# Performance work log

Measured on AMD Instinct MI355X. Metric: run time of the kernel, lower is better.

Reference implementation:

```python
import jax, jax.numpy as jnp
import numpy as np

K = 20          # knn neighbors (hard-coded default in source)
BN_EPS = 1e-3   # keras BatchNormalization default epsilon


def setup_inputs() -> dict:
    key = jax.random.key(0)
    ks = jax.random.split(key, 8)
    B, N, D = 8, 4096, 64
    x = jax.random.normal(ks[0], (B, N, D), dtype=jnp.float32)
    # Conv1D(kernel_size=1) == pointwise dense over feature dim
    w1 = jax.random.normal(ks[1], (2 * D, 32), dtype=jnp.float32) * 0.05
    b1 = jnp.zeros((32,), dtype=jnp.float32)
    g1 = jnp.ones((32,), dtype=jnp.float32)
    be1 = jnp.zeros((32,), dtype=jnp.float32)
    w2 = jax.random.normal(ks[2], (32, 64), dtype=jnp.float32) * 0.05
    b2 = jnp.zeros((64,), dtype=jnp.float32)
    g2 = jnp.ones((64,), dtype=jnp.float32)
    be2 = jnp.zeros((64,), dtype=jnp.float32)
    wd = jax.random.normal(ks[3], (64, N), dtype=jnp.float32) * 0.05
    bd = jnp.zeros((N,), dtype=jnp.float32)
    return {"x": x, "w1": w1, "b1": b1, "g1": g1, "be1": be1,
            "w2": w2, "b2": b2, "g2": g2, "be2": be2, "wd": wd, "bd": bd}


def _batchnorm(h, gamma, beta):
    # batch-stat normalization over (batch, points) axes, like BN(momentum=0) in training
    mean = jnp.mean(h, axis=(0, 1), keepdims=True)
    var = jnp.var(h, axis=(0, 1), keepdims=True)
    return gamma * (h - mean) * jax.lax.rsqrt(var + BN_EPS) + beta


def reference(x, w1, b1, g1, be1, w2, b2, g2, be2, wd, bd):
    B, N, D = x.shape
    # pairwise squared L2 distance: ||a||^2 - 2 a.b + ||b||^2  -> (B, N, N)
    inner = jnp.einsum('bnd,bmd->bnm', x, x)
    sq = jnp.sum(jnp.square(x), axis=-1, keepdims=True)  # (B, N, 1)
    adj = sq - 2.0 * inner + jnp.swapaxes(sq, 1, 2)
    # KNN: top-k of negative distance
    _, knn_idx = jax.lax.top_k(-adj, K)                   # (B, N, K)
    # gather neighbor features (B, N, K, D)
    neighbors = jax.vmap(lambda xf, idx: xf[idx])(x, knn_idx)
    central = x[:, :, None, :]                            # (B, N, 1, D)
    edge = jnp.concatenate(
        [jnp.broadcast_to(central, (B, N, K, D)), neighbors - central], axis=-1)
    feat = jnp.max(edge, axis=2)                          # (B, N, 2D)
    h = jax.nn.relu(feat @ w1 + b1)
    h = _batchnorm(h, g1, be1)
    h = jax.nn.relu(h @ w2 + b2)
    h = _batchnorm(h, g2, be2)
    pooled = jnp.max(h, axis=1)                           # (B, 64)
    return jax.nn.softmax(pooled @ wd + bd, axis=-1)      # (B, N)
```

## Files before the change

### kernel.cpp

```cpp
#include <hip/hip_runtime.h>
#include <stdint.h>

#define N_PTS 4096
#define B_SZ 8
#define D_DIM 64
#define KNN 20
#define NROWS (B_SZ * N_PTS)
#define H1C 32
#define H2C 64
#define BN_EPS 1e-3f
#define NSLICE 2
#define SLICE_C (N_PTS / NSLICE)
#define NT (SLICE_C / 64)

typedef __attribute__((ext_vector_type(8))) short bf16x8;
typedef __attribute__((ext_vector_type(4))) float f32x4;
typedef unsigned long long ull;

__device__ __forceinline__ ushort f2bf(float f) {
    uint32_t u = __float_as_uint(f);
    uint32_t r = (u + 0x7fffu + ((u >> 16) & 1u)) >> 16;
    return (ushort)r;
}
__device__ __forceinline__ float bf2f(ushort h) {
    return __uint_as_float(((uint32_t)h) << 16);
}

__device__ __forceinline__ void ins20(ull (&k)[KNN], ull cur) {
#pragma unroll
    for (int p = KNN - 1; p >= 1; --p) {
        bool c = cur < k[p - 1];
        ull t = (k[p] < cur) ? k[p] : cur;
        k[p] = c ? k[p - 1] : t;
    }
    k[0] = (k[0] < cur) ? k[0] : cur;
}

__global__ void prep_kernel(const float* __restrict__ x, ushort* __restrict__ xh,
                            ushort* __restrict__ xl, float* __restrict__ sq) {
    int row = blockIdx.x * blockDim.x + threadIdx.x;
    if (row >= NROWS) return;
    const float4* xr = (const float4*)(x + (size_t)row * D_DIM);
    ushort4* ho = (ushort4*)(xh + (size_t)row * D_DIM);
    ushort4* lo = (ushort4*)(xl + (size_t)row * D_DIM);
    float acc = 0.f;
#pragma unroll
    for (int q = 0; q < 16; ++q) {
        float4 v = xr[q];
        acc = fmaf(v.x, v.x, acc);
        acc = fmaf(v.y, v.y, acc);
        acc = fmaf(v.z, v.z, acc);
        acc = fmaf(v.w, v.w, acc);
        ushort4 h, l;
        h.x = f2bf(v.x); l.x = f2bf(v.x - bf2f(h.x));
        h.y = f2bf(v.y); l.y = f2bf(v.y - bf2f(h.y));
        h.z = f2bf(v.z); l.z = f2bf(v.z - bf2f(h.z));
        h.w = f2bf(v.w); l.w = f2bf(v.w - bf2f(h.w));
        ho[q] = h; lo[q] = l;
    }
    sq[row] = acc;
}

__global__ __launch_bounds__(256, 4) void dist_topk(
    const ushort* __restrict__ xh, const ushort* __restrict__ xl,
    const float* __restrict__ sq, ull* __restrict__ part) {
    int tid = threadIdx.x;
    int lane = tid & 63;
    int w = tid >> 6;
    int blk = blockIdx.x & 63;
    int b = blockIdx.x >> 6;
    int slice = blockIdx.y;
    const ushort* xhb = xh + (size_t)b * N_PTS * D_DIM;
    const ushort* xlb = xl + (size_t)b * N_PTS * D_DIM;
    const float* sqb = sq + (size_t)b * N_PTS;

    int qr0 = blk * 64 + w * 16;
    int fr = lane & 15;
    int fg = lane >> 4;

    bf16x8 q_h[2], q_l[2];
    {
        const ushort* ph = xhb + (size_t)(qr0 + fr) * D_DIM + fg * 8;
        const ushort* pl = xlb + (size_t)(qr0 + fr) * D_DIM + fg * 8;
        q_h[0] = *(const bf16x8*)(ph);
        q_h[1] = *(const bf16x8*)(ph + 32);
        q_l[0] = *(const bf16x8*)(pl);
        q_l[1] = *(const bf16x8*)(pl + 32);
    }
    float sqi = sqb[qr0 + fr];

    ull k20[KNN];
#pragma unroll
    for (int p = 0; p < KNN; ++p) k20[p] = ~0ull;
    ull b0 = ~0ull, b1 = ~0ull, b2 = ~0ull, b3 = ~0ull;
    ull b4 = ~0ull, b5 = ~0ull, b6 = ~0ull, b7 = ~0ull;
    int cnt = 0;
    unsigned thr = 0xFFFFFFFFu;

    int cbase = slice * SLICE_C;
    const ushort* pah = xhb + (size_t)(cbase + fr) * D_DIM + fg * 8;
    const ushort* pal = xlb + (size_t)(cbase + fr) * D_DIM + fg * 8;
    const float* psq = sqb + cbase + fg * 4;

    for (int t = 0; t < NT; ++t) {
        int c0 = cbase + t * 64;
#pragma unroll
        for (int s = 0; s < 4; ++s) {
            int cc = c0 + s * 16;
            bf16x8 a_h0 = *(const bf16x8*)(pah + s * 16 * D_DIM);
            bf16x8 a_h1 = *(const bf16x8*)(pah + s * 16 * D_DIM + 32);
            bf16x8 a_l0 = *(const bf16x8*)(pal + s * 16 * D_DIM);
            bf16x8 a_l1 = *(const bf16x8*)(pal + s * 16 * D_DIM + 32);
            float4 sqj = *(const float4*)(psq + s * 16);
            f32x4 accA = {0.f, 0.f, 0.f, 0.f};
            f32x4 accB = {0.f, 0.f, 0.f, 0.f};
            accA = __builtin_amdgcn_mfma_f32_16x16x32_bf16(a_h0, q_h[0], accA, 0, 0, 0);
            accB = __builtin_amdgcn_mfma_f32_16x16x32_bf16(a_h0, q_l[0], accB, 0, 0, 0);
            accA = __builtin_amdgcn_mfma_f32_16x16x32_bf16(a_h1, q_h[1], accA, 0, 0, 0);
            accB = __builtin_amdgcn_mfma_f32_16x16x32_bf16(a_h1, q_l[1], accB, 0, 0, 0);
            accB = __builtin_amdgcn_mfma_f32_16x16x32_bf16(a_l0, q_h[0], accB, 0, 0, 0);
            accB = __builtin_amdgcn_mfma_f32_16x16x32_bf16(a_l1, q_h[1], accB, 0, 0, 0);
            float sqjv[4] = {sqj.x, sqj.y, sqj.z, sqj.w};
#pragma unroll
            for (int qq = 0; qq < 4; ++qq) {
                float base = sqi + sqjv[qq];
                float d = fmaf(-2.f, accA[qq], fmaf(-2.f, accB[qq], base));
                d = fmaxf(d, 0.f);
                unsigned u = __float_as_uint(d);
                if (u <= thr) {
                    b7 = b6; b6 = b5; b5 = b4; b4 = b3;
                    b3 = b2; b2 = b1; b1 = b0;
                    b0 = (((ull)u) << 32) | (unsigned)(cc + fg * 4 + qq);
                    ++cnt;
                }
            }
            if (__any(cnt >= 5)) {
                ull e;
                e = (cnt >= 1) ? b0 : ~0ull; ins20(k20, e);
                e = (cnt >= 2) ? b1 : ~0ull; ins20(k20, e);
                e = (cnt >= 3) ? b2 : ~0ull; ins20(k20, e);
                e = (cnt >= 4) ? b3 : ~0ull; ins20(k20, e);
                e = (cnt >= 5) ? b4 : ~0ull; ins20(k20, e);
                if (__any(cnt >= 6)) {
                    e = (cnt >= 6) ? b5 : ~0ull; ins20(k20, e);
                    e = (cnt >= 7) ? b6 : ~0ull; ins20(k20, e);
                    e = (cnt >= 8) ? b7 : ~0ull; ins20(k20, e);
                }
                cnt = 0;
                unsigned t5  = (unsigned)(k20[4]  >> 32);
                unsigned t20 = (unsigned)(k20[19] >> 32);
                unsigned o;
                o = __shfl_xor(t5, 16);  t5  = (o > t5)  ? o : t5;
                o = __shfl_xor(t5, 32);  t5  = (o > t5)  ? o : t5;
                o = __shfl_xor(t20, 16); t20 = (o < t20) ? o : t20;
                o = __shfl_xor(t20, 32); t20 = (o < t20) ? o : t20;
                thr = (t5 < t20) ? t5 : t20;
            }
        }
        pah += 64 * D_DIM;
        pal += 64 * D_DIM;
        psq += 64;
    }
    if (__any(cnt >= 1)) {
        ull e;
        e = (cnt >= 1) ? b0 : ~0ull; ins20(k20, e);
        e = (cnt >= 2) ? b1 : ~0ull; ins20(k20, e);
        if (__any(cnt >= 3)) {
            e = (cnt >= 3) ? b2 : ~0ull; ins20(k20, e);
            e = (cnt >= 4) ? b3 : ~0ull; ins20(k20, e);
        }
    }

#pragma unroll
    for (int g = 1; g < 4; ++g) {
        for (int p = 0; p < KNN; ++p) {
            ull key = __shfl(k20[p], fr + 16 * g);
            bool useful = (lane < 16) && (key < k20[KNN - 1]);
            if (!__any(useful ? 1 : 0)) break;
            if (lane < 16) ins20(k20, key);
        }
    }
    if (lane < 16) {
        int grow = b * N_PTS + blk * 64 + w * 16 + lane;
#pragma unroll
        for (int p = 0; p < KNN; ++p)
            part[((size_t)(slice * KNN + p)) * NROWS + grow] = k20[p];
    }
}

__global__ void knn_merge(const ull* __restrict__ part, int* __restrict__ knn) {
    int row = blockIdx.x * blockDim.x + threadIdx.x;
    if (row >= NROWS) return;
    ull fin[KNN];
#pragma unroll
    for (int p = 0; p < KNN; ++p) fin[p] = part[(size_t)p * NROWS + row];
    for (int sl = 1; sl < NSLICE; ++sl) {
        for (int p = 0; p < KNN; ++p) {
            ull key = part[(size_t)(sl * KNN + p) * NROWS + row];
            if (key >= fin[KNN - 1]) break;
            ins20(fin, key);
        }
    }
#pragma unroll
    for (int q = 0; q < KNN; ++q)
        knn[(size_t)q * NROWS + row] = (int)(unsigned)(fin[q] & 0xffffffffu);
}

__global__ void edge_mlp1(const float* __restrict__ x, const int* __restrict__ knn,
                          const float* __restrict__ w1, const float* __restrict__ b1,
                          float* __restrict__ h1) {
    __shared__ float w1t[H1C][132];
    __shared__ float feat[4][128];
    int tid = threadIdx.x;
    int wave = tid >> 6, lane = tid & 63;
    for (int idx = tid; idx < 128 * H1C; idx += 256) {
        int f = idx >> 5, c = idx & 31;
        w1t[c][f] = w1[idx];
    }
    int row = blockIdx.x * 4 + wave;
    int b = row >> 12;
    int n = row & (N_PTS - 1);
    const float* xb = x + (size_t)b * N_PTS * D_DIM;
    float central = xb[(size_t)n * D_DIM + lane];
    float m = -1e30f;
    for (int k = 0; k < KNN; ++k) {
        int j = knn[(size_t)k * NROWS + row];
        float xn = xb[(size_t)j * D_DIM + lane];
        m = fmaxf(m, xn - central);
    }
    feat[wave][lane] = central;
    feat[wave][64 + lane] = m;
    __syncthreads();
    if (lane < H1C) {
        int c = lane;
        float acc = b1[c];
#pragma unroll
        for (int fq = 0; fq < 32; ++fq) {
            float4 fv = *(const float4*)(&feat[wave][fq * 4]);
            float4 wv = *(const float4*)(&w1t[c][fq * 4]);
            acc = fmaf(fv.x, wv.x, acc);
            acc = fmaf(fv.y, wv.y, acc);
            acc = fmaf(fv.z, wv.z, acc);
            acc = fmaf(fv.w, wv.w, acc);
        }
        h1[(size_t)row * H1C + c] = fmaxf(acc, 0.f);
    }
}

template <int CH>
__global__ void stats_kernel(const float* __restrict__ h, float* __restrict__ sum,
                             float* __restrict__ sumsq) {
    const int RPI = 256 / CH;
    int tid = threadIdx.x;
    int c = tid % CH;
    int r0 = tid / CH;
    float s = 0.f, s2 = 0.f;
    for (int r = blockIdx.x * RPI + r0; r < NROWS; r += gridDim.x * RPI) {
        float v = h[(size_t)r * CH + c];
        s += v;
        s2 = fmaf(v, v, s2);
    }
    __shared__ float ls[256], ls2[256];
    ls[tid] = s; ls2[tid] = s2;
    __syncthreads();
    for (int step = 128; step >= CH; step >>= 1) {
        if (tid < step) { ls[tid] += ls[tid + step]; ls2[tid] += ls2[tid + step]; }
        __syncthreads();
    }
    if (tid < CH) {
        atomicAdd(&sum[tid], ls[tid]);
        atomicAdd(&sumsq[tid], ls2[tid]);
    }
}

template <int CH>
__global__ void coeff_kernel(const float* sum, const float* sumsq, const float* g,
                             const float* be, float* a, float* cc) {
    int c = threadIdx.x;
    if (c >= CH) return;
    float mean = sum[c] * (1.f / NROWS);
    float var = sumsq[c] * (1.f / NROWS) - mean * mean;
    float aa = g[c] * rsqrtf(var + BN_EPS);
    a[c] = aa;
    cc[c] = be[c] - aa * mean;
}

__global__ void mlp2_kernel(const float* __restrict__ h1, const float* __restrict__ w2,
                            const float* __restrict__ b2, const float* __restrict__ a1,
                            const float* __restrict__ c1, float* __restrict__ h2) {
    __shared__ float w2s[H1C][H2C];
    __shared__ float hb[4][H1C];
    int tid = threadIdx.x;
    for (int idx = tid; idx < H1C * H2C; idx += 256)
        w2s[idx >> 6][idx & 63] = w2[idx];
    int rw = tid >> 6;
    int c = tid & 63;
    int row = blockIdx.x * 4 + rw;
    if (c < H1C) {
        float v = h1[(size_t)row * H1C + c];
        hb[rw][c] = fmaf(a1[c], v, c1[c]);
    }
    __syncthreads();
    float acc = b2[c];
#pragma unroll
    for (int f = 0; f < H1C; ++f)
        acc = fmaf(hb[rw][f], w2s[f][c], acc);
    h2[(size_t)row * H2C + c] = fmaxf(acc, 0.f);
}

__global__ void pool_part(const float* __restrict__ h2, float* __restrict__ pmax,
                          float* __restrict__ pmin) {
    int bb = blockIdx.x >> 6;
    int ch = blockIdx.x & 63;
    int tid = threadIdx.x;
    int rw = tid >> 6, c = tid & 63;
    float mx = -1e30f, mn = 1e30f;
    const float* hbase = h2 + (size_t)bb * N_PTS * H2C;
    for (int n = ch * 64 + rw; n < (ch + 1) * 64; n += 4) {
        float v = hbase[(size_t)n * H2C + c];
        mx = fmaxf(mx, v);
        mn = fminf(mn, v);
    }
    __shared__ float smx[256], smn[256];
    smx[tid] = mx; smn[tid] = mn;
    __syncthreads();
    if (tid < 128) { smx[tid] = fmaxf(smx[tid], smx[tid + 128]); smn[tid] = fminf(smn[tid], smn[tid + 128]); }
    __syncthreads();
    if (tid < 64) {
        pmax[((size_t)bb * 64 + ch) * 64 + tid] = fmaxf(smx[tid], smx[tid + 64]);
        pmin[((size_t)bb * 64 + ch) * 64 + tid] = fminf(smn[tid], smn[tid + 64]);
    }
}

__global__ void pool_final(const float* pmax, const float* pmin, const float* a2,
                           const float* c2, float* pooled) {
    int bb = blockIdx.x;
    int c = threadIdx.x;
    float M = -1e30f, m = 1e30f;
    for (int ch = 0; ch < 64; ++ch) {
        M = fmaxf(M, pmax[((size_t)bb * 64 + ch) * 64 + c]);
        m = fminf(m, pmin[((size_t)bb * 64 + ch) * 64 + c]);
    }
    float aa = a2[c];
    pooled[bb * 64 + c] = (aa >= 0.f) ? fmaf(aa, M, c2[c]) : fmaf(aa, m, c2[c]);
}

__global__ __launch_bounds__(256) void logits_kernel(const float* __restrict__ pooled,
                                                     const float* __restrict__ wd,
                                                     const float* __restrict__ bd,
                                                     float* __restrict__ lg) {
    __shared__ float pl[8][64];
    int tid = threadIdx.x;
    for (int i = tid; i < 8 * 64; i += 256) ((float*)pl)[i] = pooled[i];
    __syncthreads();
    int col = blockIdx.x * 64 + (tid & 63);
    int bg = tid >> 6;
    float acc0 = bd[col];
    float acc1 = acc0;
#pragma unroll
    for (int c = 0; c < 64; ++c) {
        float wv = wd[(size_t)c * N_PTS + col];
        acc0 = fmaf(pl[bg][c], wv, acc0);
        acc1 = fmaf(pl[bg + 4][c], wv, acc1);
    }
    lg[(size_t)bg * N_PTS + col] = acc0;
    lg[(size_t)(bg + 4) * N_PTS + col] = acc1;
}

__global__ __launch_bounds__(1024) void softmax_kernel(const float* __restrict__ lg,
                                                       float* __restrict__ out) {
    int bb = blockIdx.x;
    int tid = threadIdx.x;
    __shared__ float red[1024];
    float logit[4];
#pragma unroll
    for (int q = 0; q < 4; ++q)
        logit[q] = lg[(size_t)bb * N_PTS + tid + q * 1024];
    float mx = fmaxf(fmaxf(logit[0], logit[1]), fmaxf(logit[2], logit[3]));
    red[tid] = mx;
    __syncthreads();
    for (int s = 512; s >= 1; s >>= 1) {
        if (tid < s) red[tid] = fmaxf(red[tid], red[tid + s]);
        __syncthreads();
    }
    float gmax = red[0];
    __syncthreads();
    float e[4];
    float ssum = 0.f;
#pragma unroll
    for (int q = 0; q < 4; ++q) { e[q] = __expf(logit[q] - gmax); ssum += e[q]; }
    red[tid] = ssum;
    __syncthreads();
    for (int s = 512; s >= 1; s >>= 1) {
        if (tid < s) red[tid] += red[tid + s];
        __syncthreads();
    }
    float inv = 1.f / red[0];
#pragma unroll
    for (int q = 0; q < 4; ++q)
        out[(size_t)bb * N_PTS + tid + q * 1024] = e[q] * inv;
}

extern "C" void kernel_launch(void* const* d_in, const int* in_sizes, int n_in,
                              void* d_out, int out_size, void* d_ws, size_t ws_size,
                              hipStream_t stream) {
    (void)in_sizes; (void)n_in; (void)out_size; (void)ws_size;
    const float* x   = (const float*)d_in[0];
    const float* w1  = (const float*)d_in[1];
    const float* b1  = (const float*)d_in[2];
    const float* g1  = (const float*)d_in[3];
    const float* be1 = (const float*)d_in[4];
    const float* w2  = (const float*)d_in[5];
    const float* b2  = (const float*)d_in[6];
    const float* g2  = (const float*)d_in[7];
    const float* be2 = (const float*)d_in[8];
    const float* wd  = (const float*)d_in[9];
    const float* bd  = (const float*)d_in[10];

    char* ws = (char*)d_ws;
    size_t off = 0;
    auto alloc = [&](size_t bytes) -> void* {
        void* p = ws + off;
        off += (bytes + 255) & ~(size_t)255;
        return p;
    };
    ushort* xh = (ushort*)alloc((size_t)NROWS * D_DIM * 2);
    ushort* xl = (ushort*)alloc((size_t)NROWS * D_DIM * 2);
    float* sq = (float*)alloc((size_t)NROWS * 4);
    ull* part = (ull*)alloc((size_t)NROWS * NSLICE * KNN * 8);
    int* knn = (int*)alloc((size_t)NROWS * KNN * 4);
    float* h1 = (float*)alloc((size_t)NROWS * H1C * 4);
    float* h2 = (float*)alloc((size_t)NROWS * H2C * 4);
    float* stats = (float*)alloc(4096);
    float* pmax = (float*)alloc(8 * 64 * 64 * 4);
    float* pmin = (float*)alloc(8 * 64 * 64 * 4);
    float* pooled = (float*)alloc(8 * 64 * 4);
    float* lg = (float*)alloc((size_t)B_SZ * N_PTS * 4);

    float* sum1 = stats,       *sumsq1 = stats + 32, *a1 = stats + 64,  *c1 = stats + 96;
    float* sum2 = stats + 128, *sumsq2 = stats + 192, *a2 = stats + 256, *c2 = stats + 320;

    hipMemsetAsync(stats, 0, 4096, stream);

    prep_kernel<<<NROWS / 256, 256, 0, stream>>>(x, xh, xl, sq);
    dist_topk<<<dim3(B_SZ * 64, NSLICE), 256, 0, stream>>>(xh, xl, sq, part);
    knn_merge<<<NROWS / 256, 256, 0, stream>>>(part, knn);
    edge_mlp1<<<NROWS / 4, 256, 0, stream>>>(x, knn, w1, b1, h1);
    stats_kernel<H1C><<<256, 256, 0, stream>>>(h1, sum1, sumsq1);
    coeff_kernel<H1C><<<1, 32, 0, stream>>>(sum1, sumsq1, g1, be1, a1, c1);
    mlp2_kernel<<<NROWS / 4, 256, 0, stream>>>(h1, w2, b2, a1, c1, h2);
    stats_kernel<H2C><<<256, 256, 0, stream>>>(h2, sum2, sumsq2);
    coeff_kernel<H2C><<<1, 64, 0, stream>>>(sum2, sumsq2, g2, be2, a2, c2);
    pool_part<<<512, 256, 0, stream>>>(h2, pmax, pmin);
    pool_final<<<8, 64, 0, stream>>>(pmax, pmin, a2, c2, pooled);
    logits_kernel<<<64, 256, 0, stream>>>(pooled, wd, bd, lg);
    softmax_kernel<<<8, 1024, 0, stream>>>(lg, (float*)d_out);
}
```

Before: 431.2 us.

## Split candidate columns across waves within a block and merge top-k in LDS

Each block now handles 16 query rows, and its four waves each scan a quarter of the candidate points, where before each wave scanned half the points for its own rows. The per-row pruning threshold is shared through LDS via atomicMin, so one wave's progress tightens the filter for the others. The per-wave top-20 lists are merged in shared memory inside the kernel, which removes the separate knn_merge kernel and its global partial buffer. In exchange the candidate buffer is flushed on the first tile and each step reads the shared threshold, and there are four times as many blocks, each loading only 16 query rows.

```diff
diff --git a/kernel.cpp b/kernel.cpp
--- a/kernel.cpp
+++ b/kernel.cpp
@@ -9,8 +9,7 @@
 #define H1C 32
 #define H2C 64
 #define BN_EPS 1e-3f
-#define NSLICE 2
-#define SLICE_C (N_PTS / NSLICE)
+#define SLICE_C 1024
 #define NT (SLICE_C / 64)
 
 typedef __attribute__((ext_vector_type(8))) short bf16x8;
@@ -63,20 +62,24 @@
 
 __global__ __launch_bounds__(256, 4) void dist_topk(
     const ushort* __restrict__ xh, const ushort* __restrict__ xl,
-    const float* __restrict__ sq, ull* __restrict__ part) {
+    const float* __restrict__ sq, int* __restrict__ knn) {
+    __shared__ unsigned lthr[16];
+    __shared__ ull lists[4][16][KNN];
+
     int tid = threadIdx.x;
     int lane = tid & 63;
     int w = tid >> 6;
-    int blk = blockIdx.x & 63;
-    int b = blockIdx.x >> 6;
-    int slice = blockIdx.y;
+    int g = blockIdx.x;
+    int b = g >> 8;
+    int qr0 = (g & 255) * 16;
     const ushort* xhb = xh + (size_t)b * N_PTS * D_DIM;
     const ushort* xlb = xl + (size_t)b * N_PTS * D_DIM;
     const float* sqb = sq + (size_t)b * N_PTS;
 
-    int qr0 = blk * 64 + w * 16;
     int fr = lane & 15;
     int fg = lane >> 4;
+
+    if (tid < 16) lthr[tid] = 0xFFFFFFFFu;
 
     bf16x8 q_h[2], q_l[2];
     {
@@ -95,9 +98,10 @@
     ull b0 = ~0ull, b1 = ~0ull, b2 = ~0ull, b3 = ~0ull;
     ull b4 = ~0ull, b5 = ~0ull, b6 = ~0ull, b7 = ~0ull;
     int cnt = 0;
-    unsigned thr = 0xFFFFFFFFu;
-
-    int cbase = slice * SLICE_C;
+
+    __syncthreads();
+
+    int cbase = w * SLICE_C;
     const ushort* pah = xhb + (size_t)(cbase + fr) * D_DIM + fg * 8;
     const ushort* pal = xlb + (size_t)(cbase + fr) * D_DIM + fg * 8;
     const float* psq = sqb + cbase + fg * 4;
@@ -106,6 +110,7 @@
         int c0 = cbase + t * 64;
 #pragma unroll
         for (int s = 0; s < 4; ++s) {
+            unsigned thr = lthr[fr];
             int cc = c0 + s * 16;
             bf16x8 a_h0 = *(const bf16x8*)(pah + s * 16 * D_DIM);
             bf16x8 a_h1 = *(const bf16x8*)(pah + s * 16 * D_DIM + 32);
@@ -134,14 +139,14 @@
                     ++cnt;
                 }
             }
-            if (__any(cnt >= 5)) {
+            if ((t == 0) || __any(cnt >= 5)) {
                 ull e;
                 e = (cnt >= 1) ? b0 : ~0ull; ins20(k20, e);
                 e = (cnt >= 2) ? b1 : ~0ull; ins20(k20, e);
                 e = (cnt >= 3) ? b2 : ~0ull; ins20(k20, e);
                 e = (cnt >= 4) ? b3 : ~0ull; ins20(k20, e);
-                e = (cnt >= 5) ? b4 : ~0ull; ins20(k20, e);
-                if (__any(cnt >= 6)) {
+                if (__any(cnt >= 5)) {
+                    e = (cnt >= 5) ? b4 : ~0ull; ins20(k20, e);
                     e = (cnt >= 6) ? b5 : ~0ull; ins20(k20, e);
                     e = (cnt >= 7) ? b6 : ~0ull; ins20(k20, e);
                     e = (cnt >= 8) ? b7 : ~0ull; ins20(k20, e);
@@ -154,7 +159,8 @@
                 o = __shfl_xor(t5, 32);  t5  = (o > t5)  ? o : t5;
                 o = __shfl_xor(t20, 16); t20 = (o < t20) ? o : t20;
                 o = __shfl_xor(t20, 32); t20 = (o < t20) ? o : t20;
-                thr = (t5 < t20) ? t5 : t20;
+                unsigned thrloc = (t5 < t20) ? t5 : t20;
+                if (lane < 16) atomicMin(&lthr[lane], thrloc);
             }
         }
         pah += 64 * D_DIM;
@@ -172,38 +178,32 @@
     }
 
 #pragma unroll
-    for (int g = 1; g < 4; ++g) {
+    for (int gg = 1; gg < 4; ++gg) {
         for (int p = 0; p < KNN; ++p) {
-            ull key = __shfl(k20[p], fr + 16 * g);
+            ull key = __shfl(k20[p], fr + 16 * gg);
             bool useful = (lane < 16) && (key < k20[KNN - 1]);
             if (!__any(useful ? 1 : 0)) break;
             if (lane < 16) ins20(k20, key);
         }
     }
     if (lane < 16) {
-        int grow = b * N_PTS + blk * 64 + w * 16 + lane;
-#pragma unroll
-        for (int p = 0; p < KNN; ++p)
-            part[((size_t)(slice * KNN + p)) * NROWS + grow] = k20[p];
-    }
-}
-
-__global__ void knn_merge(const ull* __restrict__ part, int* __restrict__ knn) {
-    int row = blockIdx.x * blockDim.x + threadIdx.x;
-    if (row >= NROWS) return;
-    ull fin[KNN];
-#pragma unroll
-    for (int p = 0; p < KNN; ++p) fin[p] = part[(size_t)p * NROWS + row];
-    for (int sl = 1; sl < NSLICE; ++sl) {
-        for (int p = 0; p < KNN; ++p) {
-            ull key = part[(size_t)(sl * KNN + p) * NROWS + row];
-            if (key >= fin[KNN - 1]) break;
-            ins20(fin, key);
+#pragma unroll
+        for (int p = 0; p < KNN; ++p) lists[w][lane][p] = k20[p];
+    }
+    __syncthreads();
+    if (tid < 16) {
+        for (int ww = 1; ww < 4; ++ww) {
+            for (int p = 0; p < KNN; ++p) {
+                ull key = lists[ww][tid][p];
+                if (key >= k20[KNN - 1]) break;
+                ins20(k20, key);
+            }
         }
-    }
-#pragma unroll
-    for (int q = 0; q < KNN; ++q)
-        knn[(size_t)q * NROWS + row] = (int)(unsigned)(fin[q] & 0xffffffffu);
+        int grow = g * 16 + tid;
+#pragma unroll
+        for (int q = 0; q < KNN; ++q)
+            knn[(size_t)q * NROWS + grow] = (int)(unsigned)(k20[q] & 0xffffffffu);
+    }
 }
 
 __global__ void edge_mlp1(const float* __restrict__ x, const int* __restrict__ knn,
@@ -427,7 +427,6 @@
     ushort* xh = (ushort*)alloc((size_t)NROWS * D_DIM * 2);
     ushort* xl = (ushort*)alloc((size_t)NROWS * D_DIM * 2);
     float* sq = (float*)alloc((size_t)NROWS * 4);
-    ull* part = (ull*)alloc((size_t)NROWS * NSLICE * KNN * 8);
     int* knn = (int*)alloc((size_t)NROWS * KNN * 4);
     float* h1 = (float*)alloc((size_t)NROWS * H1C * 4);
     float* h2 = (float*)alloc((size_t)NROWS * H2C * 4);
@@ -443,8 +442,7 @@
     hipMemsetAsync(stats, 0, 4096, stream);
 
     prep_kernel<<<NROWS / 256, 256, 0, stream>>>(x, xh, xl, sq);
-    dist_topk<<<dim3(B_SZ * 64, NSLICE), 256, 0, stream>>>(xh, xl, sq, part);
-    knn_merge<<<NROWS / 256, 256, 0, stream>>>(part, knn);
+    dist_topk<<<NROWS / 16, 256, 0, stream>>>(xh, xl, sq, knn);
     edge_mlp1<<<NROWS / 4, 256, 0, stream>>>(x, knn, w1, b1, h1);
     stats_kernel<H1C><<<256, 256, 0, stream>>>(h1, sum1, sumsq1);
     coeff_kernel<H1C><<<1, 32, 0, stream>>>(sum1, sumsq1, g1, be1, a1, c1);
```

Result: slower. 752.0 us (+74.4%).
